# Kernel optimization log

Hardware: AMD Instinct MI355X
Metric: run time of the kernel (lower is better)

The kernel has to match this reference:

```python
import jax, jax.numpy as jnp
import numpy as np

N_NODES = 50000


def setup_inputs() -> dict:
    key = jax.random.key(0)
    k1, k2, k3, k4, k5, k6 = jax.random.split(key, 6)
    c_in, c_out = 64, 64
    n_edges = 800000
    G = jax.random.normal(k1, (N_NODES, c_in), dtype=jnp.float32)
    RSC = jax.random.normal(k2, (N_NODES, c_in), dtype=jnp.float32)
    src = jax.random.randint(k3, (n_edges,), 0, N_NODES, dtype=jnp.int64)
    dst = jax.random.randint(k4, (n_edges,), 0, N_NODES, dtype=jnp.int64)
    W = jax.random.normal(k5, (c_out, c_in), dtype=jnp.float32) / np.sqrt(c_in)
    b = jax.random.normal(k6, (c_out,), dtype=jnp.float32) * 0.01
    return {"G": G, "RSC": RSC, "src": src, "dst": dst, "W": W, "b": b}


def reference(G, RSC, src, dst, W, b):
    # Per-edge relative feature: src node 'G' feature minus dst node 'RSC' feature
    rel = G[src] - RSC[dst]                          # [E, c_in]
    # Linear + ReLU (edge MLP)
    enc = jax.nn.relu(rel @ W.T + b)                 # [E, c_out]
    # Per-dst-node reductions over variable-size mailboxes
    max_agg = jax.ops.segment_max(enc, dst, num_segments=N_NODES)  # -inf for empty
    sum_agg = jax.ops.segment_sum(enc, dst, num_segments=N_NODES)
    cnt = jax.ops.segment_sum(jnp.ones_like(dst, dtype=enc.dtype), dst,
                              num_segments=N_NODES)               # [N]
    has_mail = (cnt > 0)[:, None]
    avg_agg = sum_agg / jnp.maximum(cnt, 1.0)[:, None]
    max_agg = jnp.where(has_mail, max_agg, 0.0)      # nodes w/o edges -> 0
    # concat(max, avg) as in reduce()
    return jnp.concatenate([max_agg, avg_agg], axis=-1)  # [N, 2*c_out]
```

## Files before the change

### kernel.cpp

```cpp
#include <hip/hip_runtime.h>
#include <hip/hip_bf16.h>

#define NCH 64
#define SPAN 64
#define BIN_BLOCKS 128
#define BIN_THREADS 1024
#define HIST_BLOCKS 256
#define SORT_CAP 3072

__global__ void detect_init_kernel(const unsigned short* __restrict__ gp, int n16,
                                   const unsigned* __restrict__ ip, int niw,
                                   unsigned* __restrict__ flags,
                                   unsigned* __restrict__ gcnt, int nb) {
    if (blockIdx.x == 0) {
        __shared__ unsigned se, so;
        if (threadIdx.x == 0) { se = 0u; so = 0u; }
        __syncthreads();
        unsigned le = 0u, lo = 0u;
        for (int i = threadIdx.x; i < n16; i += blockDim.x) {
            unsigned ex = (unsigned)((gp[i] >> 7) & 0xFFu);
            if (ex >= 0xC0u) le++;
        }
        for (int i = threadIdx.x; i < niw; i += blockDim.x) {
            if ((i & 1) && ip[i] != 0u) lo++;
        }
        atomicAdd(&se, le);
        atomicAdd(&so, lo);
        __syncthreads();
        if (threadIdx.x == 0) {
            flags[0] = (se > 50u) ? 1u : 0u;
            flags[1] = (so < 50u) ? 1u : 0u;
        }
    } else {
        const int stride = (gridDim.x - 1) * blockDim.x;
        for (int i = (blockIdx.x - 1) * blockDim.x + threadIdx.x; i < nb; i += stride)
            gcnt[i] = 0u;
    }
}

__global__ void bucket_hist_kernel(const void* __restrict__ dstp,
                                   unsigned* __restrict__ gcnt,
                                   const unsigned* __restrict__ flags,
                                   int n_edges, int nb) {
    extern __shared__ unsigned lcnt[];
    for (int i = threadIdx.x; i < nb; i += blockDim.x) lcnt[i] = 0u;
    __syncthreads();
    const unsigned i64 = flags[1];
    const int stride = gridDim.x * blockDim.x;
    for (int e = blockIdx.x * blockDim.x + threadIdx.x; e < n_edges; e += stride) {
        int d = i64 ? (int)((const long long*)dstp)[e] : ((const int*)dstp)[e];
        atomicAdd(&lcnt[d >> 6], 1u);
    }
    __syncthreads();
    for (int i = threadIdx.x; i < nb; i += blockDim.x)
        if (lcnt[i]) atomicAdd(&gcnt[i], lcnt[i]);
}

__global__ void bucket_scan_kernel(const unsigned* __restrict__ gcnt,
                                   unsigned* __restrict__ boffs,
                                   unsigned* __restrict__ cursor, int nb) {
    __shared__ unsigned s[1024];
    const int t = threadIdx.x;
    const int L = (nb + 1023) / 1024;
    unsigned local = 0u;
    for (int i = 0; i < L; ++i) {
        int idx = t * L + i;
        if (idx < nb) local += gcnt[idx];
    }
    s[t] = local;
    __syncthreads();
    for (int off = 1; off < 1024; off <<= 1) {
        unsigned v = (t >= off) ? s[t - off] : 0u;
        __syncthreads();
        s[t] += v;
        __syncthreads();
    }
    unsigned run = s[t] - local;
    for (int i = 0; i < L; ++i) {
        int idx = t * L + i;
        if (idx < nb) { boffs[idx] = run; cursor[idx] = run; run += gcnt[idx]; }
    }
}

__global__ __launch_bounds__(BIN_THREADS)
void binning_kernel(const void* __restrict__ srcp, const void* __restrict__ dstp,
                    unsigned* __restrict__ cursor, unsigned* __restrict__ binned,
                    const unsigned* __restrict__ flags, int n_edges, int nb, int depth) {
    extern __shared__ unsigned lds[];
    unsigned* lcnt = lds;
    unsigned* stage = lds + nb;
    for (int i = threadIdx.x; i < nb; i += blockDim.x) lcnt[i] = 0u;
    __syncthreads();
    const unsigned i64 = flags[1];
    const int chunk = (n_edges + gridDim.x - 1) / gridDim.x;
    const int e0 = blockIdx.x * chunk;
    const int e1 = min(e0 + chunk, n_edges);
    for (int e = e0 + threadIdx.x; e < e1; e += blockDim.x) {
        int s, d;
        if (i64) {
            s = (int)((const long long*)srcp)[e];
            d = (int)((const long long*)dstp)[e];
        } else {
            s = ((const int*)srcp)[e];
            d = ((const int*)dstp)[e];
        }
        const int b = d >> 6;
        const unsigned pk = ((unsigned)(d & 63) << 26) | (unsigned)s;
        unsigned pos = atomicAdd(&lcnt[b], 1u);
        if ((int)pos < depth) {
            stage[b * depth + (int)pos] = pk;
        } else {
            unsigned g = atomicAdd(&cursor[b], 1u);
            binned[g] = pk;
        }
    }
    __syncthreads();
    for (int b = threadIdx.x; b < nb; b += blockDim.x) {
        int k = min((int)lcnt[b], depth);
        if (k > 0) {
            unsigned base = atomicAdd(&cursor[b], (unsigned)k);
            for (int i = 0; i < k; ++i) binned[base + i] = stage[b * depth + i];
        }
    }
}

__global__ __launch_bounds__(256)
void bucket_sort_kernel(const unsigned* __restrict__ binned,
                        const unsigned* __restrict__ boffs,
                        const unsigned* __restrict__ gcnt,
                        unsigned* __restrict__ sorted_src,
                        unsigned* __restrict__ offs,
                        int n_nodes, int n_edges, int nb) {
    __shared__ unsigned dcnt[SPAN];
    __shared__ unsigned doff[SPAN];
    __shared__ unsigned cur[SPAN];
    __shared__ unsigned stage[SORT_CAP];
    const int b = blockIdx.x;
    const int tid = threadIdx.x;
    const int estart = (int)boffs[b];
    const int count = (int)gcnt[b];

    if (tid < SPAN) dcnt[tid] = 0u;
    __syncthreads();

    for (int i = tid; i < count; i += 256) {
        const unsigned pk = binned[estart + i];
        atomicAdd(&dcnt[pk >> 26], 1u);
        if (i < SORT_CAP) stage[i] = pk;
    }
    __syncthreads();

    if (tid == 0) {
        unsigned run = 0u;
        #pragma unroll
        for (int i = 0; i < SPAN; ++i) { doff[i] = run; cur[i] = run; run += dcnt[i]; }
    }
    __syncthreads();

    if (tid < SPAN) {
        const int n = b * SPAN + tid;
        if (n < n_nodes) offs[n] = (unsigned)estart + doff[tid];
    }
    if (b == nb - 1 && tid == 0) offs[n_nodes] = (unsigned)n_edges;

    const int lim = (count < SORT_CAP) ? count : SORT_CAP;
    for (int i = tid; i < lim; i += 256) {
        const unsigned pk = stage[i];
        const unsigned pos = atomicAdd(&cur[pk >> 26], 1u);
        sorted_src[estart + pos] = pk & 0x03FFFFFFu;
    }
    for (int i = SORT_CAP + tid; i < count; i += 256) {
        const unsigned pk = binned[estart + i];
        const unsigned pos = atomicAdd(&cur[pk >> 26], 1u);
        sorted_src[estart + pos] = pk & 0x03FFFFFFu;
    }
}

__global__ void gemm2_kernel(const void* __restrict__ Gp, const void* __restrict__ Rp,
                             const void* __restrict__ Wp, const void* __restrict__ bp,
                             void* __restrict__ PQ,
                             const unsigned* __restrict__ flags, int n_nodes) {
    const unsigned f32 = flags[0];
    const int lane = threadIdx.x & 63;
    const int waveInBlk = threadIdx.x >> 6;
    const int wavesPerBlk = blockDim.x >> 6;
    const int gwave = blockIdx.x * wavesPerBlk + waveInBlk;
    const int nwaves = gridDim.x * wavesPerBlk;
    const int n_rows = 2 * n_nodes;
    const int ngroups = (n_rows + 3) / 4;

    __shared__ float ldsb[4 * 4 * NCH];
    float* slot = &ldsb[waveInBlk * 4 * NCH];

    float w[NCH];
    float bias;
    if (f32) {
        const float* Wf = (const float*)Wp;
        #pragma unroll
        for (int k = 0; k < NCH; ++k) w[k] = Wf[lane * NCH + k];
        bias = ((const float*)bp)[lane];
    } else {
        const __hip_bfloat16* Wh = (const __hip_bfloat16*)Wp;
        #pragma unroll
        for (int k = 0; k < NCH; ++k) w[k] = __bfloat162float(Wh[lane * NCH + k]);
        bias = __bfloat162float(((const __hip_bfloat16*)bp)[lane]);
    }

    const int niter = (ngroups + nwaves - 1) / nwaves;
    for (int it = 0; it < niter; ++it) {
        const int grp = gwave + it * nwaves;
        const bool gvalid = (grp < ngroups);
        const int m0 = grp * 4;
        if (gvalid) {
            const int myrow = m0 + (lane >> 4);
            const int col = (lane & 15) * 4;
            float x0 = 0.f, x1 = 0.f, x2 = 0.f, x3 = 0.f;
            if (myrow < n_rows) {
                const bool isQ = (myrow >= n_nodes);
                const int r = isQ ? (myrow - n_nodes) : myrow;
                const void* inp = isQ ? Rp : Gp;
                if (f32) {
                    float4 v = *(const float4*)((const float*)inp + (size_t)r * NCH + col);
                    x0 = v.x; x1 = v.y; x2 = v.z; x3 = v.w;
                } else {
                    ushort4 v = *(const ushort4*)((const unsigned short*)inp +
                                                  (size_t)r * NCH + col);
                    x0 = __bfloat162float(*(__hip_bfloat16*)&v.x);
                    x1 = __bfloat162float(*(__hip_bfloat16*)&v.y);
                    x2 = __bfloat162float(*(__hip_bfloat16*)&v.z);
                    x3 = __bfloat162float(*(__hip_bfloat16*)&v.w);
                }
            }
            const int sb = (lane >> 4) * NCH + col;
            slot[sb + 0] = x0; slot[sb + 1] = x1; slot[sb + 2] = x2; slot[sb + 3] = x3;
        }
        __syncthreads();
        if (gvalid) {
            #pragma unroll
            for (int rr = 0; rr < 4; ++rr) {
                const int m = m0 + rr;
                if (m < n_rows) {
                    float a0 = 0.f, a1 = 0.f, a2 = 0.f, a3 = 0.f;
                    const float4* r4 = (const float4*)(slot + rr * NCH);
                    #pragma unroll
                    for (int q = 0; q < 16; ++q) {
                        float4 rv = r4[q];
                        a0 = fmaf(rv.x, w[4 * q + 0], a0);
                        a1 = fmaf(rv.y, w[4 * q + 1], a1);
                        a2 = fmaf(rv.z, w[4 * q + 2], a2);
                        a3 = fmaf(rv.w, w[4 * q + 3], a3);
                    }
                    float acc = (a0 + a1) + (a2 + a3);
                    if (m >= n_nodes) acc -= bias;
                    if (f32) ((float*)PQ)[(size_t)m * NCH + lane] = acc;
                    else ((__hip_bfloat16*)PQ)[(size_t)m * NCH + lane] =
                             __float2bfloat16(acc);
                }
            }
        }
        __syncthreads();
    }
}

__global__ void node_kernel(const void* __restrict__ PQ,
                            const unsigned* __restrict__ sorted_src,
                            const unsigned* __restrict__ offs,
                            const unsigned* __restrict__ flags,
                            void* __restrict__ outp, int n_nodes) {
    const unsigned f32 = flags[0];
    const int lane = threadIdx.x & 63;
    const int gwave = (blockIdx.x * blockDim.x + threadIdx.x) >> 6;
    const int nwaves = (gridDim.x * blockDim.x) >> 6;
    const float* Pf = (const float*)PQ;
    const unsigned short* Ph = (const unsigned short*)PQ;

    for (int n = gwave; n < n_nodes; n += nwaves) {
        float q;
        if (f32) q = Pf[(size_t)(n_nodes + n) * NCH + lane];
        else {
            unsigned short h = Ph[(size_t)(n_nodes + n) * NCH + lane];
            q = __bfloat162float(*(__hip_bfloat16*)&h);
        }
        const int start = (int)offs[n];
        const int end = (int)offs[n + 1];
        float vmax = 0.0f, vsum = 0.0f;
        int j = start;
        for (; j + 4 <= end; j += 4) {
            const int s0 = (int)sorted_src[j];
            const int s1 = (int)sorted_src[j + 1];
            const int s2 = (int)sorted_src[j + 2];
            const int s3 = (int)sorted_src[j + 3];
            float p0, p1, p2, p3;
            if (f32) {
                p0 = Pf[(size_t)s0 * NCH + lane];
                p1 = Pf[(size_t)s1 * NCH + lane];
                p2 = Pf[(size_t)s2 * NCH + lane];
                p3 = Pf[(size_t)s3 * NCH + lane];
            } else {
                unsigned short h0 = Ph[(size_t)s0 * NCH + lane];
                unsigned short h1 = Ph[(size_t)s1 * NCH + lane];
                unsigned short h2 = Ph[(size_t)s2 * NCH + lane];
                unsigned short h3 = Ph[(size_t)s3 * NCH + lane];
                p0 = __bfloat162float(*(__hip_bfloat16*)&h0);
                p1 = __bfloat162float(*(__hip_bfloat16*)&h1);
                p2 = __bfloat162float(*(__hip_bfloat16*)&h2);
                p3 = __bfloat162float(*(__hip_bfloat16*)&h3);
            }
            const float v0 = fmaxf(p0 - q, 0.0f);
            const float v1 = fmaxf(p1 - q, 0.0f);
            const float v2 = fmaxf(p2 - q, 0.0f);
            const float v3 = fmaxf(p3 - q, 0.0f);
            vmax = fmaxf(fmaxf(vmax, v0), fmaxf(v1, fmaxf(v2, v3)));
            vsum += (v0 + v1) + (v2 + v3);
        }
        for (; j < end; ++j) {
            const int s = (int)sorted_src[j];
            float p;
            if (f32) p = Pf[(size_t)s * NCH + lane];
            else {
                unsigned short h = Ph[(size_t)s * NCH + lane];
                p = __bfloat162float(*(__hip_bfloat16*)&h);
            }
            const float v = fmaxf(p - q, 0.0f);
            vmax = fmaxf(vmax, v);
            vsum += v;
        }
        const int deg = end - start;
        const float avg = vsum / (float)(deg > 0 ? deg : 1);
        if (f32) {
            float* out = (float*)outp;
            out[(size_t)n * 2 * NCH + lane] = vmax;
            out[(size_t)n * 2 * NCH + NCH + lane] = avg;
        } else {
            __hip_bfloat16* out = (__hip_bfloat16*)outp;
            out[(size_t)n * 2 * NCH + lane] = __float2bfloat16(vmax);
            out[(size_t)n * 2 * NCH + NCH + lane] = __float2bfloat16(avg);
        }
    }
}

extern "C" void kernel_launch(void* const* d_in, const int* in_sizes, int n_in,
                              void* d_out, int out_size, void* d_ws, size_t ws_size,
                              hipStream_t stream) {
    const void* G = d_in[0];
    const void* RSC = d_in[1];
    const void* src = d_in[2];
    const void* dst = d_in[3];
    const void* W = d_in[4];
    const void* b = d_in[5];

    const int n_nodes = in_sizes[0] / NCH;
    const int n_edges = in_sizes[2];
    const int nb = (n_nodes + SPAN - 1) / SPAN;

    char* ws = (char*)d_ws;
    unsigned* flags = (unsigned*)ws;
    size_t off = 256;
    unsigned* binned = (unsigned*)(ws + off);
    off += (((size_t)n_edges * 4 + 255) / 256) * 256;
    unsigned* sorted_src = (unsigned*)(ws + off);
    off += (((size_t)n_edges * 4 + 255) / 256) * 256;
    unsigned* offs = (unsigned*)(ws + off);
    off += (((size_t)(n_nodes + 1) * 4 + 255) / 256) * 256;
    unsigned* boffs = (unsigned*)(ws + off);
    off += (((size_t)nb * 4 + 255) / 256) * 256;
    unsigned* cursor = (unsigned*)(ws + off);
    off += (((size_t)nb * 4 + 255) / 256) * 256;
    unsigned* gcnt = (unsigned*)(ws + off);
    off += (((size_t)nb * 4 + 255) / 256) * 256;
    void* PQ = (void*)(ws + off);

    const int n_g_probe = (in_sizes[0] < 8192) ? in_sizes[0] : 8192;
    const int n_idx_probe = (n_edges < 8192) ? n_edges : 8192;

    detect_init_kernel<<<64, 256, 0, stream>>>((const unsigned short*)G, n_g_probe,
                                               (const unsigned*)src, n_idx_probe,
                                               flags, gcnt, nb);

    bucket_hist_kernel<<<HIST_BLOCKS, 256, (size_t)nb * 4, stream>>>(
        dst, gcnt, flags, n_edges, nb);

    bucket_scan_kernel<<<1, 1024, 0, stream>>>(gcnt, boffs, cursor, nb);

    int depth = 16384 / nb - 1;
    if (depth > 19) depth = 19;
    if (depth < 4) depth = 4;
    const size_t bin_lds = (size_t)nb * (depth + 1) * 4;
    binning_kernel<<<BIN_BLOCKS, BIN_THREADS, bin_lds, stream>>>(
        src, dst, cursor, binned, flags, n_edges, nb, depth);

    bucket_sort_kernel<<<nb, 256, 0, stream>>>(binned, boffs, gcnt, sorted_src,
                                               offs, n_nodes, n_edges, nb);

    gemm2_kernel<<<2048, 256, 0, stream>>>(G, RSC, W, b, PQ, flags, n_nodes);

    node_kernel<<<2048, 256, 0, stream>>>(PQ, sorted_src, offs, flags, d_out, n_nodes);
}
```

Before: 199.9 us.

## Fold dtype detection into histogram, add MFMA bf16 GEMM path, unroll gather loop

```diff
diff --git a/kernel.cpp b/kernel.cpp
--- a/kernel.cpp
+++ b/kernel.cpp
@@ -8,44 +8,40 @@
 #define HIST_BLOCKS 256
 #define SORT_CAP 3072
 
-__global__ void detect_init_kernel(const unsigned short* __restrict__ gp, int n16,
+using bf16x8 = __attribute__((ext_vector_type(8))) short;
+using f32x4 = __attribute__((ext_vector_type(4))) float;
+
+__global__ void bucket_hist_kernel(const void* __restrict__ dstp,
+                                   const unsigned short* __restrict__ gp, int n16,
                                    const unsigned* __restrict__ ip, int niw,
                                    unsigned* __restrict__ flags,
-                                   unsigned* __restrict__ gcnt, int nb) {
+                                   unsigned* __restrict__ gcnt,
+                                   int n_edges, int nb) {
+    extern __shared__ unsigned lcnt[];
+    unsigned* sodd = &lcnt[nb];
+    for (int i = threadIdx.x; i < nb; i += blockDim.x) lcnt[i] = 0u;
+    if (threadIdx.x == 0) *sodd = 0u;
+    __syncthreads();
+    unsigned lo = 0u;
+    for (int i = threadIdx.x; i < niw; i += blockDim.x)
+        if ((i & 1) && ip[i] != 0u) lo++;
+    atomicAdd(sodd, lo);
+    __syncthreads();
+    const unsigned i64 = (*sodd < 50u) ? 1u : 0u;
+    if (blockIdx.x == 0 && threadIdx.x == 0) flags[1] = i64;
     if (blockIdx.x == 0) {
-        __shared__ unsigned se, so;
-        if (threadIdx.x == 0) { se = 0u; so = 0u; }
-        __syncthreads();
-        unsigned le = 0u, lo = 0u;
+        unsigned le = 0u;
         for (int i = threadIdx.x; i < n16; i += blockDim.x) {
             unsigned ex = (unsigned)((gp[i] >> 7) & 0xFFu);
             if (ex >= 0xC0u) le++;
         }
-        for (int i = threadIdx.x; i < niw; i += blockDim.x) {
-            if ((i & 1) && ip[i] != 0u) lo++;
-        }
-        atomicAdd(&se, le);
-        atomicAdd(&so, lo);
-        __syncthreads();
-        if (threadIdx.x == 0) {
-            flags[0] = (se > 50u) ? 1u : 0u;
-            flags[1] = (so < 50u) ? 1u : 0u;
-        }
-    } else {
-        const int stride = (gridDim.x - 1) * blockDim.x;
-        for (int i = (blockIdx.x - 1) * blockDim.x + threadIdx.x; i < nb; i += stride)
-            gcnt[i] = 0u;
-    }
-}
-
-__global__ void bucket_hist_kernel(const void* __restrict__ dstp,
-                                   unsigned* __restrict__ gcnt,
-                                   const unsigned* __restrict__ flags,
-                                   int n_edges, int nb) {
-    extern __shared__ unsigned lcnt[];
-    for (int i = threadIdx.x; i < nb; i += blockDim.x) lcnt[i] = 0u;
-    __syncthreads();
-    const unsigned i64 = flags[1];
+        __syncthreads();
+        if (threadIdx.x == 0) *sodd = 0u;
+        __syncthreads();
+        atomicAdd(sodd, le);
+        __syncthreads();
+        if (threadIdx.x == 0) flags[0] = (*sodd > 50u) ? 1u : 0u;
+    }
     const int stride = gridDim.x * blockDim.x;
     for (int e = blockIdx.x * blockDim.x + threadIdx.x; e < n_edges; e += stride) {
         int d = i64 ? (int)((const long long*)dstp)[e] : ((const int*)dstp)[e];
@@ -176,35 +172,85 @@
     }
 }
 
-__global__ void gemm2_kernel(const void* __restrict__ Gp, const void* __restrict__ Rp,
-                             const void* __restrict__ Wp, const void* __restrict__ bp,
-                             void* __restrict__ PQ,
-                             const unsigned* __restrict__ flags, int n_nodes) {
+__global__ __launch_bounds__(256)
+void gemm2_kernel(const void* __restrict__ Gp, const void* __restrict__ Rp,
+                  const void* __restrict__ Wp, const void* __restrict__ bp,
+                  void* __restrict__ PQ,
+                  const unsigned* __restrict__ flags, int n_nodes) {
     const unsigned f32 = flags[0];
     const int lane = threadIdx.x & 63;
+    const int n_rows = 2 * n_nodes;
+
+    if (!f32) {
+        const unsigned short* Gh = (const unsigned short*)Gp;
+        const unsigned short* Rh = (const unsigned short*)Rp;
+        const unsigned short* Wh = (const unsigned short*)Wp;
+        const __hip_bfloat16* bh = (const __hip_bfloat16*)bp;
+        __hip_bfloat16* out = (__hip_bfloat16*)PQ;
+        const int q = lane >> 4;
+        const int mr = lane & 15;
+        const int gwave = (blockIdx.x * blockDim.x + threadIdx.x) >> 6;
+        const int nwaves = (gridDim.x * blockDim.x) >> 6;
+        const int ngrp = (n_rows + 15) / 16;
+
+        bf16x8 Bf[4][2];
+        float bv[4];
+        #pragma unroll
+        for (int t = 0; t < 4; ++t) {
+            const int c = t * 16 + mr;
+            Bf[t][0] = *(const bf16x8*)(const void*)(Wh + (size_t)c * NCH + q * 8);
+            Bf[t][1] = *(const bf16x8*)(const void*)(Wh + (size_t)c * NCH + 32 + q * 8);
+            bv[t] = __bfloat162float(bh[c]);
+        }
+
+        for (int grp = gwave; grp < ngrp; grp += nwaves) {
+            const int m0 = grp * 16;
+            int arow = m0 + mr;
+            if (arow >= n_rows) arow = n_rows - 1;
+            const unsigned short* ap = (arow < n_nodes)
+                ? Gh + (size_t)arow * NCH
+                : Rh + (size_t)(arow - n_nodes) * NCH;
+            const bf16x8 A0 = *(const bf16x8*)(const void*)(ap + q * 8);
+            const bf16x8 A1 = *(const bf16x8*)(const void*)(ap + 32 + q * 8);
+            f32x4 acc0 = {0.f, 0.f, 0.f, 0.f}, acc1 = acc0, acc2 = acc0, acc3 = acc0;
+            acc0 = __builtin_amdgcn_mfma_f32_16x16x32_bf16(A0, Bf[0][0], acc0, 0, 0, 0);
+            acc1 = __builtin_amdgcn_mfma_f32_16x16x32_bf16(A0, Bf[1][0], acc1, 0, 0, 0);
+            acc2 = __builtin_amdgcn_mfma_f32_16x16x32_bf16(A0, Bf[2][0], acc2, 0, 0, 0);
+            acc3 = __builtin_amdgcn_mfma_f32_16x16x32_bf16(A0, Bf[3][0], acc3, 0, 0, 0);
+            acc0 = __builtin_amdgcn_mfma_f32_16x16x32_bf16(A1, Bf[0][1], acc0, 0, 0, 0);
+            acc1 = __builtin_amdgcn_mfma_f32_16x16x32_bf16(A1, Bf[1][1], acc1, 0, 0, 0);
+            acc2 = __builtin_amdgcn_mfma_f32_16x16x32_bf16(A1, Bf[2][1], acc2, 0, 0, 0);
+            acc3 = __builtin_amdgcn_mfma_f32_16x16x32_bf16(A1, Bf[3][1], acc3, 0, 0, 0);
+            #pragma unroll
+            for (int r = 0; r < 4; ++r) {
+                const int row = m0 + q * 4 + r;
+                if (row < n_rows) {
+                    const bool isQ = (row >= n_nodes);
+                    const size_t rb = (size_t)row * NCH + mr;
+                    out[rb +  0] = __float2bfloat16(acc0[r] - (isQ ? bv[0] : 0.f));
+                    out[rb + 16] = __float2bfloat16(acc1[r] - (isQ ? bv[1] : 0.f));
+                    out[rb + 32] = __float2bfloat16(acc2[r] - (isQ ? bv[2] : 0.f));
+                    out[rb + 48] = __float2bfloat16(acc3[r] - (isQ ? bv[3] : 0.f));
+                }
+            }
+        }
+        return;
+    }
+
     const int waveInBlk = threadIdx.x >> 6;
     const int wavesPerBlk = blockDim.x >> 6;
     const int gwave = blockIdx.x * wavesPerBlk + waveInBlk;
     const int nwaves = gridDim.x * wavesPerBlk;
-    const int n_rows = 2 * n_nodes;
     const int ngroups = (n_rows + 3) / 4;
 
     __shared__ float ldsb[4 * 4 * NCH];
     float* slot = &ldsb[waveInBlk * 4 * NCH];
 
     float w[NCH];
-    float bias;
-    if (f32) {
-        const float* Wf = (const float*)Wp;
-        #pragma unroll
-        for (int k = 0; k < NCH; ++k) w[k] = Wf[lane * NCH + k];
-        bias = ((const float*)bp)[lane];
-    } else {
-        const __hip_bfloat16* Wh = (const __hip_bfloat16*)Wp;
-        #pragma unroll
-        for (int k = 0; k < NCH; ++k) w[k] = __bfloat162float(Wh[lane * NCH + k]);
-        bias = __bfloat162float(((const __hip_bfloat16*)bp)[lane]);
-    }
+    const float* Wf = (const float*)Wp;
+    #pragma unroll
+    for (int k = 0; k < NCH; ++k) w[k] = Wf[lane * NCH + k];
+    const float bias = ((const float*)bp)[lane];
 
     const int niter = (ngroups + nwaves - 1) / nwaves;
     for (int it = 0; it < niter; ++it) {
@@ -218,18 +264,9 @@
             if (myrow < n_rows) {
                 const bool isQ = (myrow >= n_nodes);
                 const int r = isQ ? (myrow - n_nodes) : myrow;
-                const void* inp = isQ ? Rp : Gp;
-                if (f32) {
-                    float4 v = *(const float4*)((const float*)inp + (size_t)r * NCH + col);
-                    x0 = v.x; x1 = v.y; x2 = v.z; x3 = v.w;
-                } else {
-                    ushort4 v = *(const ushort4*)((const unsigned short*)inp +
-                                                  (size_t)r * NCH + col);
-                    x0 = __bfloat162float(*(__hip_bfloat16*)&v.x);
-                    x1 = __bfloat162float(*(__hip_bfloat16*)&v.y);
-                    x2 = __bfloat162float(*(__hip_bfloat16*)&v.z);
-                    x3 = __bfloat162float(*(__hip_bfloat16*)&v.w);
-                }
+                const float* inp = (const float*)(isQ ? Rp : Gp);
+                float4 v = *(const float4*)(inp + (size_t)r * NCH + col);
+                x0 = v.x; x1 = v.y; x2 = v.z; x3 = v.w;
             }
             const int sb = (lane >> 4) * NCH + col;
             slot[sb + 0] = x0; slot[sb + 1] = x1; slot[sb + 2] = x2; slot[sb + 3] = x3;
@@ -243,18 +280,16 @@
                     float a0 = 0.f, a1 = 0.f, a2 = 0.f, a3 = 0.f;
                     const float4* r4 = (const float4*)(slot + rr * NCH);
                     #pragma unroll
-                    for (int q = 0; q < 16; ++q) {
-                        float4 rv = r4[q];
-                        a0 = fmaf(rv.x, w[4 * q + 0], a0);
-                        a1 = fmaf(rv.y, w[4 * q + 1], a1);
-                        a2 = fmaf(rv.z, w[4 * q + 2], a2);
-                        a3 = fmaf(rv.w, w[4 * q + 3], a3);
+                    for (int qq = 0; qq < 16; ++qq) {
+                        float4 rv = r4[qq];
+                        a0 = fmaf(rv.x, w[4 * qq + 0], a0);
+                        a1 = fmaf(rv.y, w[4 * qq + 1], a1);
+                        a2 = fmaf(rv.z, w[4 * qq + 2], a2);
+                        a3 = fmaf(rv.w, w[4 * qq + 3], a3);
                     }
                     float acc = (a0 + a1) + (a2 + a3);
                     if (m >= n_nodes) acc -= bias;
-                    if (f32) ((float*)PQ)[(size_t)m * NCH + lane] = acc;
-                    else ((__hip_bfloat16*)PQ)[(size_t)m * NCH + lane] =
-                             __float2bfloat16(acc);
+                    ((float*)PQ)[(size_t)m * NCH + lane] = acc;
                 }
             }
         }
@@ -285,33 +320,27 @@
         const int end = (int)offs[n + 1];
         float vmax = 0.0f, vsum = 0.0f;
         int j = start;
-        for (; j + 4 <= end; j += 4) {
-            const int s0 = (int)sorted_src[j];
-            const int s1 = (int)sorted_src[j + 1];
-            const int s2 = (int)sorted_src[j + 2];
-            const int s3 = (int)sorted_src[j + 3];
-            float p0, p1, p2, p3;
+        for (; j + 8 <= end; j += 8) {
+            int s[8];
+            #pragma unroll
+            for (int u = 0; u < 8; ++u) s[u] = (int)sorted_src[j + u];
+            float p[8];
             if (f32) {
-                p0 = Pf[(size_t)s0 * NCH + lane];
-                p1 = Pf[(size_t)s1 * NCH + lane];
-                p2 = Pf[(size_t)s2 * NCH + lane];
-                p3 = Pf[(size_t)s3 * NCH + lane];
+                #pragma unroll
+                for (int u = 0; u < 8; ++u) p[u] = Pf[(size_t)s[u] * NCH + lane];
             } else {
-                unsigned short h0 = Ph[(size_t)s0 * NCH + lane];
-                unsigned short h1 = Ph[(size_t)s1 * NCH + lane];
-                unsigned short h2 = Ph[(size_t)s2 * NCH + lane];
-                unsigned short h3 = Ph[(size_t)s3 * NCH + lane];
-                p0 = __bfloat162float(*(__hip_bfloat16*)&h0);
-                p1 = __bfloat162float(*(__hip_bfloat16*)&h1);
-                p2 = __bfloat162float(*(__hip_bfloat16*)&h2);
-                p3 = __bfloat162float(*(__hip_bfloat16*)&h3);
-            }
-            const float v0 = fmaxf(p0 - q, 0.0f);
-            const float v1 = fmaxf(p1 - q, 0.0f);
-            const float v2 = fmaxf(p2 - q, 0.0f);
-            const float v3 = fmaxf(p3 - q, 0.0f);
-            vmax = fmaxf(fmaxf(vmax, v0), fmaxf(v1, fmaxf(v2, v3)));
-            vsum += (v0 + v1) + (v2 + v3);
+                unsigned short h[8];
+                #pragma unroll
+                for (int u = 0; u < 8; ++u) h[u] = Ph[(size_t)s[u] * NCH + lane];
+                #pragma unroll
+                for (int u = 0; u < 8; ++u) p[u] = __bfloat162float(*(__hip_bfloat16*)&h[u]);
+            }
+            #pragma unroll
+            for (int u = 0; u < 8; ++u) {
+                const float v = fmaxf(p[u] - q, 0.0f);
+                vmax = fmaxf(vmax, v);
+                vsum += v;
+            }
         }
         for (; j < end; ++j) {
             const int s = (int)sorted_src[j];
@@ -373,12 +402,11 @@
     const int n_g_probe = (in_sizes[0] < 8192) ? in_sizes[0] : 8192;
     const int n_idx_probe = (n_edges < 8192) ? n_edges : 8192;
 
-    detect_init_kernel<<<64, 256, 0, stream>>>((const unsigned short*)G, n_g_probe,
-                                               (const unsigned*)src, n_idx_probe,
-                                               flags, gcnt, nb);
-
-    bucket_hist_kernel<<<HIST_BLOCKS, 256, (size_t)nb * 4, stream>>>(
-        dst, gcnt, flags, n_edges, nb);
+    hipMemsetAsync(gcnt, 0, (size_t)nb * 4, stream);
+
+    bucket_hist_kernel<<<HIST_BLOCKS, 256, (size_t)(nb + 1) * 4, stream>>>(
+        dst, (const unsigned short*)G, n_g_probe, (const unsigned*)src, n_idx_probe,
+        flags, gcnt, n_edges, nb);
 
     bucket_scan_kernel<<<1, 1024, 0, stream>>>(gcnt, boffs, cursor, nb);
 
@@ -392,7 +420,8 @@
     bucket_sort_kernel<<<nb, 256, 0, stream>>>(binned, boffs, gcnt, sorted_src,
                                                offs, n_nodes, n_edges, nb);
 
-    gemm2_kernel<<<2048, 256, 0, stream>>>(G, RSC, W, b, PQ, flags, n_nodes);
+    const int ngrp = (2 * n_nodes + 15) / 16;
+    gemm2_kernel<<<(ngrp + 3) / 4, 256, 0, stream>>>(G, RSC, W, b, PQ, flags, n_nodes);
 
     node_kernel<<<2048, 256, 0, stream>>>(PQ, sorted_src, offs, flags, d_out, n_nodes);
 }
```

Measured after the change: 211.8 us. 5.9% more time.
